# Kernel optimization log

Hardware: AMD Instinct MI355X
Metric: run time of the kernel (lower is better)

## Reference

```python
import jax, jax.numpy as jnp
import numpy as np

VOCAB = 32000
HID = 1024
BATCH = 8
SEQ = 512


def setup_inputs() -> dict:
    key = jax.random.key(0)
    k1, k2, k3, k4 = jax.random.split(key, 4)
    scale = 1.0 / np.sqrt(HID)
    return {
        "batched_sequence_ids": jax.random.randint(k1, (BATCH, SEQ), 0, VOCAB, dtype=jnp.int32),
        "w_out": jax.random.normal(k2, (HID, VOCAB), dtype=jnp.float32) * scale,
        "b_out": jnp.zeros((VOCAB,), dtype=jnp.float32),
        "W_ih": jax.random.normal(k3, (HID, 4 * HID), dtype=jnp.float32) * scale,
        "W_hh": jax.random.normal(k4, (HID, 4 * HID), dtype=jnp.float32) * scale,
        "b_lstm": jnp.zeros((4 * HID,), dtype=jnp.float32),
    }


def _lstm_scan(x_gates, W_hh):
    # x_gates: [B, S, 4H] = precomputed input contribution + bias
    B = x_gates.shape[0]
    H = W_hh.shape[0]
    h0 = jnp.zeros((B, H), dtype=x_gates.dtype)
    c0 = jnp.zeros((B, H), dtype=x_gates.dtype)

    def step(carry, xg_t):
        h, c = carry
        gates = xg_t + h @ W_hh  # [B, 4H]
        i, f, g, o = jnp.split(gates, 4, axis=-1)
        i = jax.nn.sigmoid(i)
        f = jax.nn.sigmoid(f)
        g = jnp.tanh(g)
        o = jax.nn.sigmoid(o)
        c_new = f * c + i * g
        h_new = o * jnp.tanh(c_new)
        return (h_new, c_new), h_new

    # scan over time axis: move S to leading dim
    (_, _), hs = jax.lax.scan(step, (h0, c0), jnp.swapaxes(x_gates, 0, 1))
    return jnp.swapaxes(hs, 0, 1)  # [B, S, H]


def reference(batched_sequence_ids, w_out, b_out, W_ih, W_hh, b_lstm):
    # weight-tied embedding lookup: w_out is [H, V]; emb = w_out[:, ids].T
    emb = jnp.take(w_out.T, batched_sequence_ids, axis=0)  # [B, S, H]
    # precompute input-to-gate contribution for all timesteps in one GEMM
    x_gates = jnp.einsum('bsh,hg->bsg', emb, W_ih) + b_lstm  # [B, S, 4H]
    hs = _lstm_scan(x_gates, W_hh)  # [B, S, H]
    logits = jnp.einsum('bsh,hv->bsv', hs, w_out) + b_out  # [B, S, V]
    return logits
```

## Files before the change

### kernel.cpp

```cpp
#include <hip/hip_runtime.h>
#include <math.h>

#define VOCAB 32000
#define HID   1024
#define BATCH 8
#define SEQ   512
#define GD    (4*HID)
#define ROWS  (BATCH*SEQ)

typedef __attribute__((ext_vector_type(8))) short short8;
typedef __attribute__((ext_vector_type(4))) float f32x4;

__device__ __forceinline__ float hi_f32(float x) {
    return __uint_as_float(__float_as_uint(x) & 0xFFFF0000u);
}
__device__ __forceinline__ unsigned pack_pair(float x) {
    unsigned hb = __float_as_uint(x) & 0xFFFF0000u;
    float lo = x - __uint_as_float(hb);
    return hb | (__float_as_uint(lo) >> 16);
}
__device__ __forceinline__ unsigned pack_hi2(float x, float y) {
    return (__float_as_uint(x) >> 16) | (__float_as_uint(y) & 0xFFFF0000u);
}

__device__ __forceinline__ void gload16(const void* g, void* l) {
    __builtin_amdgcn_global_load_lds(
        (__attribute__((address_space(1))) void*)g,
        (__attribute__((address_space(3))) void*)l, 16, 0, 0);
}

__global__ __launch_bounds__(256) void k_gather_split(const int* __restrict__ ids,
                                                      const float* __restrict__ w_out,
                                                      unsigned short* __restrict__ emb_hi,
                                                      unsigned short* __restrict__ emb_lo)
{
    int row = blockIdx.x;
    int id  = ids[row];
    const float* src = w_out + id;
    for (int h = threadIdx.x; h < HID; h += 256) {
        float v  = src[(size_t)h * VOCAB];
        float lo = v - hi_f32(v);
        emb_hi[(size_t)row*HID + h] = (unsigned short)(__float_as_uint(v)  >> 16);
        emb_lo[(size_t)row*HID + h] = (unsigned short)(__float_as_uint(lo) >> 16);
    }
}

__global__ __launch_bounds__(256) void k_transpose(const float* __restrict__ W,
                                                   float* __restrict__ WT)
{
    __shared__ float tile[32][33];
    int tx = threadIdx.x, ty = threadIdx.y;
    int x = blockIdx.x*32 + tx;
    int y = blockIdx.y*32 + ty;
    #pragma unroll
    for (int i = 0; i < 32; i += 8)
        tile[ty + i][tx] = W[(size_t)(y + i)*GD + x];
    __syncthreads();
    int k   = blockIdx.y*32 + tx;
    int col = blockIdx.x*32 + ty;
    #pragma unroll
    for (int i = 0; i < 32; i += 8)
        WT[(size_t)(col + i)*HID + k] = tile[tx][ty + i];
}

__global__ __launch_bounds__(256) void k_transsplit(const float* __restrict__ W,
                                                    unsigned short* __restrict__ hiT,
                                                    unsigned short* __restrict__ loT,
                                                    int N)
{
    __shared__ float tile[32][33];
    int tx = threadIdx.x, ty = threadIdx.y;
    int x = blockIdx.x*32 + tx;
    int y = blockIdx.y*32 + ty;
    #pragma unroll
    for (int i = 0; i < 32; i += 8)
        tile[ty + i][tx] = W[(size_t)(y + i)*N + x];
    __syncthreads();
    int n = blockIdx.x*32 + ty;
    int k = blockIdx.y*32 + tx;
    #pragma unroll
    for (int i = 0; i < 32; i += 8) {
        float v  = tile[tx][ty + i];
        float lo = v - hi_f32(v);
        hiT[(size_t)(n + i)*HID + k] = (unsigned short)(__float_as_uint(v)  >> 16);
        loT[(size_t)(n + i)*HID + k] = (unsigned short)(__float_as_uint(lo) >> 16);
    }
}

__global__ __launch_bounds__(256) void k_split_f32(const float* __restrict__ src,
                                                   unsigned short* __restrict__ hi,
                                                   unsigned short* __restrict__ lo,
                                                   long n4)
{
    long i0 = (long)blockIdx.x * 256 + threadIdx.x;
    long stride = (long)gridDim.x * 256;
    for (long i = i0; i < n4; i += stride) {
        float4 v = ((const float4*)src)[i];
        unsigned h0 = __float_as_uint(v.x) >> 16, h1 = __float_as_uint(v.y) >> 16;
        unsigned h2 = __float_as_uint(v.z) >> 16, h3 = __float_as_uint(v.w) >> 16;
        unsigned l0 = __float_as_uint(v.x - hi_f32(v.x)) >> 16;
        unsigned l1 = __float_as_uint(v.y - hi_f32(v.y)) >> 16;
        unsigned l2 = __float_as_uint(v.z - hi_f32(v.z)) >> 16;
        unsigned l3 = __float_as_uint(v.w - hi_f32(v.w)) >> 16;
        ((uint2*)hi)[i] = make_uint2(h0 | (h1 << 16), h2 | (h3 << 16));
        ((uint2*)lo)[i] = make_uint2(l0 | (l1 << 16), l2 | (l3 << 16));
    }
}

#define GBM 128
#define GBN 128
#define GBK 32

__global__ __launch_bounds__(256) void k_gemm_fast(
    const unsigned short* __restrict__ Ah,  const unsigned short* __restrict__ Al,
    const unsigned short* __restrict__ BhT, const unsigned short* __restrict__ BlT,
    const float* __restrict__ bias, float* __restrict__ C,
    int M, int N, int K)
{
    __shared__ __align__(16) unsigned short lds[4][4096];

    const int tid  = threadIdx.x;
    const int lane = tid & 63;
    const int wid  = tid >> 6;
    const int wm = wid >> 1, wn = wid & 1;
    const int l15 = lane & 15, l4 = lane >> 4;
    const int brow = blockIdx.y * GBM;
    const int bcol = blockIdx.x * GBN;

    const int lhi  = lane >> 3;
    const int c8   = (lane & 7) ^ lhi;
    const int koff = (c8 & 3) * 8;
    const int r0   = 32*wid + 2*lhi + (c8 >> 2);
    const int r1   = r0 + 16;
    const size_t a0 = (size_t)(brow + r0)*K + koff;
    const size_t a1 = (size_t)(brow + r1)*K + koff;
    const size_t b0 = (size_t)(bcol + r0)*K + koff;
    const size_t b1 = (size_t)(bcol + r1)*K + koff;
    char* lbase = (char*)&lds[0][0];
    const int cb0 = wid*2048, cb1 = wid*2048 + 1024;

    const int ra = wm*64 + l15;
    const int ga = ra >> 1;
    const int abyte = ga*128 + (((((ra & 1) << 2) | l4) ^ (ga & 7)) << 4);
    const int rb = wn*64 + l15;
    const int gb = rb >> 1;
    const int bbyte = gb*128 + (((((rb & 1) << 2) | l4) ^ (gb & 7)) << 4);

    f32x4 acc[4][4] = {};

    for (int k0 = 0; k0 < K; k0 += GBK) {
        gload16(Ah  + a0 + k0, lbase         + cb0);
        gload16(Ah  + a1 + k0, lbase         + cb1);
        gload16(Al  + a0 + k0, lbase + 8192  + cb0);
        gload16(Al  + a1 + k0, lbase + 8192  + cb1);
        gload16(BhT + b0 + k0, lbase + 16384 + cb0);
        gload16(BhT + b1 + k0, lbase + 16384 + cb1);
        gload16(BlT + b0 + k0, lbase + 24576 + cb0);
        gload16(BlT + b1 + k0, lbase + 24576 + cb1);
        __syncthreads();

        short8 ah[4], al[4], bh[4], bl[4];
        #pragma unroll
        for (int m = 0; m < 4; ++m) {
            ah[m] = *(const short8*)(lbase         + abyte + m*1024);
            al[m] = *(const short8*)(lbase + 8192  + abyte + m*1024);
        }
        #pragma unroll
        for (int n = 0; n < 4; ++n) {
            bh[n] = *(const short8*)(lbase + 16384 + bbyte + n*1024);
            bl[n] = *(const short8*)(lbase + 24576 + bbyte + n*1024);
        }
        #pragma unroll
        for (int n = 0; n < 4; ++n)
            #pragma unroll
            for (int m = 0; m < 4; ++m) {
                acc[m][n] = __builtin_amdgcn_mfma_f32_16x16x32_bf16(ah[m], bh[n], acc[m][n], 0, 0, 0);
                acc[m][n] = __builtin_amdgcn_mfma_f32_16x16x32_bf16(ah[m], bl[n], acc[m][n], 0, 0, 0);
                acc[m][n] = __builtin_amdgcn_mfma_f32_16x16x32_bf16(al[m], bh[n], acc[m][n], 0, 0, 0);
            }
        __syncthreads();
    }

    #pragma unroll
    for (int n = 0; n < 4; ++n) {
        int col = bcol + wn*64 + n*16 + l15;
        float bv = bias[col];
        #pragma unroll
        for (int m = 0; m < 4; ++m) {
            int rbs = brow + wm*64 + m*16 + l4*4;
            #pragma unroll
            for (int r = 0; r < 4; ++r)
                C[(size_t)(rbs + r)*N + col] = acc[m][n][r] + bv;
        }
    }
}

__global__ __launch_bounds__(256) void k_gemm_mfma(const float* __restrict__ A,
                                                   const float* __restrict__ B,
                                                   const float* __restrict__ bias,
                                                   float* __restrict__ C,
                                                   int M, int N, int K)
{
    __shared__ unsigned short As_hi[GBM][40];
    __shared__ unsigned short As_lo[GBM][40];
    __shared__ unsigned int   Bs[GBK][130];

    int tid  = threadIdx.x;
    int brow = blockIdx.y * GBM;
    int bcol = blockIdx.x * GBN;

    int lane = tid & 63;
    int wid  = tid >> 6;
    int wm   = wid >> 1;
    int wn   = wid & 1;
    int l15  = lane & 15;
    int l4   = lane >> 4;

    int a_m = tid >> 3;
    int a_c = tid & 7;
    int b_k = tid >> 5;
    int b_n = tid & 31;

    f32x4 acc[4][4] = {};

    for (int k0 = 0; k0 < K; k0 += GBK) {
        #pragma unroll
        for (int p = 0; p < 4; ++p) {
            int r = a_m + p*32;
            float4 v = *(const float4*)(A + (size_t)(brow + r)*K + k0 + a_c*4);
            unsigned h0 = pack_hi2(v.x, v.y);
            unsigned h1 = pack_hi2(v.z, v.w);
            float lx = v.x - hi_f32(v.x);
            float ly = v.y - hi_f32(v.y);
            float lz = v.z - hi_f32(v.z);
            float lw = v.w - hi_f32(v.w);
            unsigned l0 = pack_hi2(lx, ly);
            unsigned l1 = pack_hi2(lz, lw);
            *(uint2*)&As_hi[r][a_c*4] = make_uint2(h0, h1);
            *(uint2*)&As_lo[r][a_c*4] = make_uint2(l0, l1);
        }
        #pragma unroll
        for (int p = 0; p < 4; ++p) {
            int kk = b_k + p*8;
            float4 v = *(const float4*)(B + (size_t)(k0 + kk)*N + bcol + b_n*4);
            unsigned w0 = pack_pair(v.x);
            unsigned w1 = pack_pair(v.y);
            unsigned w2 = pack_pair(v.z);
            unsigned w3 = pack_pair(v.w);
            *(uint2*)&Bs[kk][b_n*4]     = make_uint2(w0, w1);
            *(uint2*)&Bs[kk][b_n*4 + 2] = make_uint2(w2, w3);
        }
        __syncthreads();

        short8 ah[4], al[4];
        #pragma unroll
        for (int m = 0; m < 4; ++m) {
            int r = wm*64 + m*16 + l15;
            ah[m] = *(const short8*)&As_hi[r][l4*8];
            al[m] = *(const short8*)&As_lo[r][l4*8];
        }

        #pragma unroll
        for (int n = 0; n < 4; ++n) {
            int col = wn*64 + n*16 + l15;
            unsigned w[8];
            #pragma unroll
            for (int j = 0; j < 8; ++j)
                w[j] = Bs[l4*8 + j][col];
            union { short8 v; unsigned d[4]; } bh, bl;
            #pragma unroll
            for (int d = 0; d < 4; ++d) {
                bh.d[d] = (w[2*d] >> 16)      | (w[2*d+1] & 0xFFFF0000u);
                bl.d[d] = (w[2*d] & 0xFFFFu)  | (w[2*d+1] << 16);
            }
            #pragma unroll
            for (int m = 0; m < 4; ++m) {
                acc[m][n] = __builtin_amdgcn_mfma_f32_16x16x32_bf16(ah[m], bh.v, acc[m][n], 0, 0, 0);
                acc[m][n] = __builtin_amdgcn_mfma_f32_16x16x32_bf16(ah[m], bl.v, acc[m][n], 0, 0, 0);
                acc[m][n] = __builtin_amdgcn_mfma_f32_16x16x32_bf16(al[m], bh.v, acc[m][n], 0, 0, 0);
            }
        }
        __syncthreads();
    }

    #pragma unroll
    for (int n = 0; n < 4; ++n) {
        int col = bcol + wn*64 + n*16 + l15;
        float bv = bias[col];
        #pragma unroll
        for (int m = 0; m < 4; ++m) {
            int rb = brow + wm*64 + m*16 + l4*4;
            #pragma unroll
            for (int r = 0; r < 4; ++r)
                C[(size_t)(rb + r)*N + col] = acc[m][n][r] + bv;
        }
    }
}

__global__ __launch_bounds__(256) void k_lstm_step(const float* __restrict__ xg,
                                                   const float* __restrict__ WT,
                                                   float* __restrict__ c_state,
                                                   float* __restrict__ hs,
                                                   int t)
{
    int j    = blockIdx.x;
    int gate = threadIdx.x >> 6;
    int lane = threadIdx.x & 63;
    int col  = gate*HID + j;

    float acc[8] = {};
    if (t > 0) {
        const float4* wv = (const float4*)(WT + (size_t)col*HID);
        #pragma unroll
        for (int c = 0; c < 4; ++c) {
            int k4 = c*64 + lane;
            float4 w4 = wv[k4];
            #pragma unroll
            for (int b = 0; b < 8; ++b) {
                float4 h4 = ((const float4*)(hs + ((size_t)b*SEQ + (t-1))*HID))[k4];
                acc[b] += w4.x*h4.x + w4.y*h4.y + w4.z*h4.z + w4.w*h4.w;
            }
        }
        #pragma unroll
        for (int b = 0; b < 8; ++b) {
            acc[b] += __shfl_xor(acc[b], 32);
            acc[b] += __shfl_xor(acc[b], 16);
            acc[b] += __shfl_xor(acc[b], 8);
            acc[b] += __shfl_xor(acc[b], 4);
            acc[b] += __shfl_xor(acc[b], 2);
            acc[b] += __shfl_xor(acc[b], 1);
        }
    }

    __shared__ float g_sm[4][8];
    if (lane == 0) {
        #pragma unroll
        for (int b = 0; b < 8; ++b)
            g_sm[gate][b] = acc[b];
    }
    __syncthreads();

    if (threadIdx.x < 8) {
        int b = threadIdx.x;
        size_t xbase = ((size_t)b*SEQ + t)*GD + j;
        float iv = g_sm[0][b] + xg[xbase];
        float fv = g_sm[1][b] + xg[xbase + HID];
        float gv = g_sm[2][b] + xg[xbase + 2*HID];
        float ov = g_sm[3][b] + xg[xbase + 3*HID];
        iv = 1.0f / (1.0f + expf(-iv));
        fv = 1.0f / (1.0f + expf(-fv));
        gv = tanhf(gv);
        ov = 1.0f / (1.0f + expf(-ov));
        float c  = (t > 0) ? c_state[(size_t)b*HID + j] : 0.0f;
        float cn = fv*c + iv*gv;
        float hn = ov * tanhf(cn);
        c_state[(size_t)b*HID + j] = cn;
        hs[((size_t)b*SEQ + t)*HID + j] = hn;
    }
}

extern "C" void kernel_launch(void* const* d_in, const int* in_sizes, int n_in,
                              void* d_out, int out_size, void* d_ws, size_t ws_size,
                              hipStream_t stream)
{
    const int*   ids    = (const int*)  d_in[0];
    const float* w_out  = (const float*)d_in[1];
    const float* b_out  = (const float*)d_in[2];
    const float* W_ih   = (const float*)d_in[3];
    const float* W_hh   = (const float*)d_in[4];
    const float* b_lstm = (const float*)d_in[5];
    float* out = (float*)d_out;

    char* ob = (char*)d_out;
    unsigned short* emb_hi  = (unsigned short*)(ob);
    unsigned short* emb_lo  = (unsigned short*)(ob + 8388608);
    float*          WT      = (float*)(ob + 16777216);
    float*          xg      = (float*)(ob + 33554432);
    float*          cstate  = (float*)(ob + 100663296);
    unsigned short* wih_hiT = (unsigned short*)(ob + 100696064);
    unsigned short* wih_loT = (unsigned short*)(ob + 109084672);
    float*          hs_dout = (float*)(ob + 117473280);

    char* wb = (char*)d_ws;
    const size_t NEED = 147849216ull;
    const bool big_ws = (ws_size >= NEED);
    unsigned short* hs_hi  = (unsigned short*)(wb);
    unsigned short* hs_lo  = (unsigned short*)(wb + 8388608);
    unsigned short* wo_hiT = (unsigned short*)(wb + 16777216);
    unsigned short* wo_loT = (unsigned short*)(wb + 82313216);
    float* hs = big_ws ? hs_dout : (float*)wb;

    k_gather_split<<<ROWS, 256, 0, stream>>>(ids, w_out, emb_hi, emb_lo);

    k_transpose<<<dim3(GD/32, HID/32), dim3(32, 8), 0, stream>>>(W_hh, WT);

    k_transsplit<<<dim3(GD/32, HID/32), dim3(32, 8), 0, stream>>>(
        W_ih, wih_hiT, wih_loT, GD);

    k_gemm_fast<<<dim3(GD/GBN, ROWS/GBM), 256, 0, stream>>>(
        emb_hi, emb_lo, wih_hiT, wih_loT, b_lstm, xg, ROWS, GD, HID);

    for (int t = 0; t < SEQ; ++t)
        k_lstm_step<<<HID, 256, 0, stream>>>(xg, WT, cstate, hs, t);

    if (big_ws) {
        k_transsplit<<<dim3(VOCAB/32, HID/32), dim3(32, 8), 0, stream>>>(
            w_out, wo_hiT, wo_loT, VOCAB);
        k_split_f32<<<1024, 256, 0, stream>>>(hs, hs_hi, hs_lo, (long)ROWS*HID/4);
        k_gemm_fast<<<dim3(VOCAB/GBN, ROWS/GBM), 256, 0, stream>>>(
            hs_hi, hs_lo, wo_hiT, wo_loT, b_out, out, ROWS, VOCAB, HID);
    } else {
        k_gemm_mfma<<<dim3(VOCAB/GBN, ROWS/GBM), 256, 0, stream>>>(
            hs, w_out, b_out, out, ROWS, VOCAB, HID);
    }
}
```

Before: 5.221 ms.

## Replace per-timestep LSTM launches with persistent flag-synchronized scan kernel using MFMA

Replaces 512 separate per-timestep kernel launches with one persistent kernel of 64 blocks that loops over time and synchronizes across blocks with per-block flags in global memory and a double-buffered hidden state. The recurrent matmul now uses bf16 hi/lo split MFMA instructions on a transposed, split W_hh instead of fp32 FMA dot products, and the cell state stays in registers. This is meant to remove launch overhead and global round trips per step. It relies on all 64 blocks being co-resident and on relaxed atomics for inter-block visibility, and the three-term bf16 split can give slightly different numerics.

```diff
diff --git a/kernel.cpp b/kernel.cpp
--- a/kernel.cpp
+++ b/kernel.cpp
@@ -7,6 +7,7 @@
 #define SEQ   512
 #define GD    (4*HID)
 #define ROWS  (BATCH*SEQ)
+#define SNB   64
 
 typedef __attribute__((ext_vector_type(8))) short short8;
 typedef __attribute__((ext_vector_type(4))) float f32x4;
@@ -43,24 +44,6 @@
         emb_hi[(size_t)row*HID + h] = (unsigned short)(__float_as_uint(v)  >> 16);
         emb_lo[(size_t)row*HID + h] = (unsigned short)(__float_as_uint(lo) >> 16);
     }
-}
-
-__global__ __launch_bounds__(256) void k_transpose(const float* __restrict__ W,
-                                                   float* __restrict__ WT)
-{
-    __shared__ float tile[32][33];
-    int tx = threadIdx.x, ty = threadIdx.y;
-    int x = blockIdx.x*32 + tx;
-    int y = blockIdx.y*32 + ty;
-    #pragma unroll
-    for (int i = 0; i < 32; i += 8)
-        tile[ty + i][tx] = W[(size_t)(y + i)*GD + x];
-    __syncthreads();
-    int k   = blockIdx.y*32 + tx;
-    int col = blockIdx.x*32 + ty;
-    #pragma unroll
-    for (int i = 0; i < 32; i += 8)
-        WT[(size_t)(col + i)*HID + k] = tile[tx][ty + i];
 }
 
 __global__ __launch_bounds__(256) void k_transsplit(const float* __restrict__ W,
@@ -297,65 +280,125 @@
     }
 }
 
-__global__ __launch_bounds__(256) void k_lstm_step(const float* __restrict__ xg,
-                                                   const float* __restrict__ WT,
-                                                   float* __restrict__ c_state,
-                                                   float* __restrict__ hs,
-                                                   int t)
-{
-    int j    = blockIdx.x;
-    int gate = threadIdx.x >> 6;
-    int lane = threadIdx.x & 63;
-    int col  = gate*HID + j;
-
-    float acc[8] = {};
-    if (t > 0) {
-        const float4* wv = (const float4*)(WT + (size_t)col*HID);
-        #pragma unroll
-        for (int c = 0; c < 4; ++c) {
-            int k4 = c*64 + lane;
-            float4 w4 = wv[k4];
-            #pragma unroll
-            for (int b = 0; b < 8; ++b) {
-                float4 h4 = ((const float4*)(hs + ((size_t)b*SEQ + (t-1))*HID))[k4];
-                acc[b] += w4.x*h4.x + w4.y*h4.y + w4.z*h4.z + w4.w*h4.w;
-            }
-        }
-        #pragma unroll
-        for (int b = 0; b < 8; ++b) {
-            acc[b] += __shfl_xor(acc[b], 32);
-            acc[b] += __shfl_xor(acc[b], 16);
-            acc[b] += __shfl_xor(acc[b], 8);
-            acc[b] += __shfl_xor(acc[b], 4);
-            acc[b] += __shfl_xor(acc[b], 2);
-            acc[b] += __shfl_xor(acc[b], 1);
-        }
-    }
-
-    __shared__ float g_sm[4][8];
-    if (lane == 0) {
-        #pragma unroll
-        for (int b = 0; b < 8; ++b)
-            g_sm[gate][b] = acc[b];
-    }
-    __syncthreads();
-
-    if (threadIdx.x < 8) {
-        int b = threadIdx.x;
-        size_t xbase = ((size_t)b*SEQ + t)*GD + j;
-        float iv = g_sm[0][b] + xg[xbase];
-        float fv = g_sm[1][b] + xg[xbase + HID];
-        float gv = g_sm[2][b] + xg[xbase + 2*HID];
-        float ov = g_sm[3][b] + xg[xbase + 3*HID];
-        iv = 1.0f / (1.0f + expf(-iv));
-        fv = 1.0f / (1.0f + expf(-fv));
-        gv = tanhf(gv);
-        ov = 1.0f / (1.0f + expf(-ov));
-        float c  = (t > 0) ? c_state[(size_t)b*HID + j] : 0.0f;
-        float cn = fv*c + iv*gv;
-        float hn = ov * tanhf(cn);
-        c_state[(size_t)b*HID + j] = cn;
-        hs[((size_t)b*SEQ + t)*HID + j] = hn;
+__global__ __launch_bounds__(256) void k_lstm_scan(
+    const float* __restrict__ xg,
+    const unsigned short* __restrict__ WhT_hi,
+    const unsigned short* __restrict__ WhT_lo,
+    unsigned int* __restrict__ hbuf,
+    unsigned int* __restrict__ flags,
+    float* __restrict__ hs)
+{
+    __shared__ unsigned int h_lds[8][1028];
+    __shared__ float g_sm[4][16][16];
+
+    const int tid  = threadIdx.x;
+    const int lane = tid & 63;
+    const int w    = tid >> 6;
+    const int l15  = lane & 15;
+    const int l4   = lane >> 4;
+    const int j0   = blockIdx.x * 16;
+
+    const unsigned short* wh = WhT_hi + (size_t)(w*HID + j0 + l15)*HID + l4*8;
+    const unsigned short* wl = WhT_lo + (size_t)(w*HID + j0 + l15)*HID + l4*8;
+
+    const int tb = tid & 7;
+    const int tj = tid >> 3;
+    float creg = 0.0f;
+
+    for (int t = 0; t < SEQ; ++t) {
+        float xv0 = 0, xv1 = 0, xv2 = 0, xv3 = 0;
+        if (tid < 128) {
+            size_t xb = ((size_t)tb*SEQ + t)*GD + j0 + tj;
+            xv0 = xg[xb];
+            xv1 = xg[xb + HID];
+            xv2 = xg[xb + 2*HID];
+            xv3 = xg[xb + 3*HID];
+        }
+
+        if (t > 0) {
+            if (w == 0) {
+                while (__hip_atomic_load(&flags[lane], __ATOMIC_RELAXED,
+                                         __HIP_MEMORY_SCOPE_AGENT) < (unsigned)t)
+                    __builtin_amdgcn_s_sleep(1);
+            }
+            __syncthreads();
+
+            unsigned int* hp = hbuf + ((t - 1) & 1) * (8 * 1024);
+            #pragma unroll
+            for (int i = 0; i < 32; ++i) {
+                int idx = i * 256 + tid;
+                h_lds[idx >> 10][idx & 1023] =
+                    __hip_atomic_load(hp + idx, __ATOMIC_RELAXED,
+                                      __HIP_MEMORY_SCOPE_AGENT);
+            }
+            __syncthreads();
+
+            const unsigned int* hrow = &h_lds[l15 & 7][0];
+            f32x4 acc0 = {}, acc1 = {};
+            #pragma unroll
+            for (int ks = 0; ks < 32; ks += 2) {
+                uint4 p0a = *(const uint4*)(hrow + ks*32 + l4*8);
+                uint4 p0b = *(const uint4*)(hrow + ks*32 + l4*8 + 4);
+                uint4 p1a = *(const uint4*)(hrow + (ks+1)*32 + l4*8);
+                uint4 p1b = *(const uint4*)(hrow + (ks+1)*32 + l4*8 + 4);
+                union { short8 v; unsigned d[4]; } ah0, al0, ah1, al1;
+                unsigned q0[8] = {p0a.x,p0a.y,p0a.z,p0a.w,p0b.x,p0b.y,p0b.z,p0b.w};
+                unsigned q1[8] = {p1a.x,p1a.y,p1a.z,p1a.w,p1b.x,p1b.y,p1b.z,p1b.w};
+                #pragma unroll
+                for (int d = 0; d < 4; ++d) {
+                    ah0.d[d] = (q0[2*d] >> 16)     | (q0[2*d+1] & 0xFFFF0000u);
+                    al0.d[d] = (q0[2*d] & 0xFFFFu) | (q0[2*d+1] << 16);
+                    ah1.d[d] = (q1[2*d] >> 16)     | (q1[2*d+1] & 0xFFFF0000u);
+                    al1.d[d] = (q1[2*d] & 0xFFFFu) | (q1[2*d+1] << 16);
+                }
+                short8 bh0 = *(const short8*)(wh + ks*32);
+                short8 bl0 = *(const short8*)(wl + ks*32);
+                short8 bh1 = *(const short8*)(wh + (ks+1)*32);
+                short8 bl1 = *(const short8*)(wl + (ks+1)*32);
+                acc0 = __builtin_amdgcn_mfma_f32_16x16x32_bf16(ah0.v, bh0, acc0, 0, 0, 0);
+                acc1 = __builtin_amdgcn_mfma_f32_16x16x32_bf16(ah1.v, bh1, acc1, 0, 0, 0);
+                acc0 = __builtin_amdgcn_mfma_f32_16x16x32_bf16(ah0.v, bl0, acc0, 0, 0, 0);
+                acc1 = __builtin_amdgcn_mfma_f32_16x16x32_bf16(ah1.v, bl1, acc1, 0, 0, 0);
+                acc0 = __builtin_amdgcn_mfma_f32_16x16x32_bf16(al0.v, bh0, acc0, 0, 0, 0);
+                acc1 = __builtin_amdgcn_mfma_f32_16x16x32_bf16(al1.v, bh1, acc1, 0, 0, 0);
+            }
+            f32x4 acc = acc0 + acc1;
+            *(f32x4*)&g_sm[w][l15][l4*4] = acc;
+        }
+        __syncthreads();
+
+        if (tid < 128) {
+            float s0 = 0, s1 = 0, s2 = 0, s3 = 0;
+            if (t > 0) {
+                s0 = g_sm[0][tj][tb];
+                s1 = g_sm[1][tj][tb];
+                s2 = g_sm[2][tj][tb];
+                s3 = g_sm[3][tj][tb];
+            }
+            float iv = s0 + xv0;
+            float fv = s1 + xv1;
+            float gv = s2 + xv2;
+            float ov = s3 + xv3;
+            iv = 1.0f / (1.0f + expf(-iv));
+            fv = 1.0f / (1.0f + expf(-fv));
+            gv = tanhf(gv);
+            ov = 1.0f / (1.0f + expf(-ov));
+            float cn = fv*creg + iv*gv;
+            creg = cn;
+            float hn = ov * tanhf(cn);
+            int jc = j0 + tj;
+            hs[((size_t)tb*SEQ + t)*HID + jc] = hn;
+            unsigned hb2 = __float_as_uint(hn) & 0xFFFF0000u;
+            unsigned pk  = hb2 |
+                (__float_as_uint(hn - __uint_as_float(hb2)) >> 16);
+            __hip_atomic_store(hbuf + (t & 1)*(8*1024) + (size_t)tb*1024 + jc,
+                               pk, __ATOMIC_RELAXED, __HIP_MEMORY_SCOPE_AGENT);
+        }
+        __syncthreads();
+
+        if (t < SEQ - 1 && tid == 0)
+            __hip_atomic_store(&flags[blockIdx.x], (unsigned)(t + 1),
+                               __ATOMIC_RELAXED, __HIP_MEMORY_SCOPE_AGENT);
     }
 }
 
@@ -374,12 +417,14 @@
     char* ob = (char*)d_out;
     unsigned short* emb_hi  = (unsigned short*)(ob);
     unsigned short* emb_lo  = (unsigned short*)(ob + 8388608);
-    float*          WT      = (float*)(ob + 16777216);
+    unsigned short* whh_hiT = (unsigned short*)(ob + 16777216);
+    unsigned short* whh_loT = (unsigned short*)(ob + 25165824);
     float*          xg      = (float*)(ob + 33554432);
-    float*          cstate  = (float*)(ob + 100663296);
-    unsigned short* wih_hiT = (unsigned short*)(ob + 100696064);
-    unsigned short* wih_loT = (unsigned short*)(ob + 109084672);
-    float*          hs_dout = (float*)(ob + 117473280);
+    unsigned int*   hbuf    = (unsigned int*)(ob + 100663296);
+    unsigned int*   flags   = (unsigned int*)(ob + 100728832);
+    unsigned short* wih_hiT = (unsigned short*)(ob + 100732928);
+    unsigned short* wih_loT = (unsigned short*)(ob + 109121536);
+    float*          hs_dout = (float*)(ob + 117510144);
 
     char* wb = (char*)d_ws;
     const size_t NEED = 147849216ull;
@@ -392,7 +437,8 @@
 
     k_gather_split<<<ROWS, 256, 0, stream>>>(ids, w_out, emb_hi, emb_lo);
 
-    k_transpose<<<dim3(GD/32, HID/32), dim3(32, 8), 0, stream>>>(W_hh, WT);
+    k_transsplit<<<dim3(GD/32, HID/32), dim3(32, 8), 0, stream>>>(
+        W_hh, whh_hiT, whh_loT, GD);
 
     k_transsplit<<<dim3(GD/32, HID/32), dim3(32, 8), 0, stream>>>(
         W_ih, wih_hiT, wih_loT, GD);
@@ -400,8 +446,9 @@
     k_gemm_fast<<<dim3(GD/GBN, ROWS/GBM), 256, 0, stream>>>(
         emb_hi, emb_lo, wih_hiT, wih_loT, b_lstm, xg, ROWS, GD, HID);
 
-    for (int t = 0; t < SEQ; ++t)
-        k_lstm_step<<<HID, 256, 0, stream>>>(xg, WT, cstate, hs, t);
+    hipMemsetAsync((void*)flags, 0, SNB * sizeof(unsigned int), stream);
+    k_lstm_scan<<<SNB, 256, 0, stream>>>(
+        xg, whh_hiT, whh_loT, hbuf, flags, hs);
 
     if (big_ws) {
         k_transsplit<<<dim3(VOCAB/32, HID/32), dim3(32, 8), 0, stream>>>(
```

After: 9.627 ms. 1.84x slower.
